# Kernel optimization log

Measured on AMD Instinct MI355X. Metric: run time of the kernel, lower is better.

The kernel has to match this reference:

```python
import jax, jax.numpy as jnp
import numpy as np

H = 1024  # hidden_size
NH = 16   # num_attention_heads
HD = H // NH  # head_dim = 64


def setup_inputs() -> dict:
    key = jax.random.key(0)
    ks = jax.random.split(key, 9)
    s = 0.02
    return {
        "hidden_states": jax.random.normal(ks[0], (2, 2048, H), dtype=jnp.float32),
        "Wq": jax.random.normal(ks[1], (H, H), dtype=jnp.float32) * s,
        "bq": jnp.zeros((H,), dtype=jnp.float32),
        "Wk": jax.random.normal(ks[2], (H, H), dtype=jnp.float32) * s,
        "bk": jnp.zeros((H,), dtype=jnp.float32),
        "Wv": jax.random.normal(ks[3], (H, H), dtype=jnp.float32) * s,
        "bv": jnp.zeros((H,), dtype=jnp.float32),
        "Wo": jax.random.normal(ks[4], (H, H), dtype=jnp.float32) * s,
        "bo": jnp.zeros((H,), dtype=jnp.float32),
    }


def reference(hidden_states, Wq, bq, Wk, bk, Wv, bv, Wo, bo):
    B, S, _ = hidden_states.shape
    scale = 1.0 / np.sqrt(HD)
    # torch Linear: x @ W.T + b
    q = (hidden_states @ Wq.T + bq).reshape(B, S, NH, HD).transpose(0, 2, 1, 3)
    k = (hidden_states @ Wk.T + bk).reshape(B, S, NH, HD).transpose(0, 2, 1, 3)
    v = (hidden_states @ Wv.T + bv).reshape(B, S, NH, HD).transpose(0, 2, 1, 3)
    # full (non-causal) attention; tiled_matmul == plain matmul mathematically
    scores = jnp.einsum("bhqd,bhkd->bhqk", q, k) * scale
    attn = jax.nn.softmax(scores, axis=-1)
    out = jnp.einsum("bhqk,bhkd->bhqd", attn, v)
    out = out.transpose(0, 2, 1, 3).reshape(B, S, H)
    return out @ Wo.T + bo
```

## Files before the change

kernel.cpp:

```cpp
#include <hip/hip_runtime.h>

typedef unsigned short u16;
typedef __attribute__((ext_vector_type(8))) short bf16x8;
typedef __attribute__((ext_vector_type(4))) float f32x4;
typedef __attribute__((ext_vector_type(4))) unsigned int u32x4;

#define SEQ 2048
#define HID 1024
#define NHEAD 16
#define HDIM 64
#define MTOK 4096

#define MFMA16(a,b,c) __builtin_amdgcn_mfma_f32_16x16x32_bf16(a,b,c,0,0,0)

__device__ __forceinline__ u16 f2bf(float f){
  unsigned int u = __builtin_bit_cast(unsigned int, f);
  u += 0x7fffu + ((u >> 16) & 1u);
  return (u16)(u >> 16);
}

__device__ __forceinline__ void gload16(const u16* g, u16* l){
  __builtin_amdgcn_global_load_lds((const __attribute__((address_space(1))) void*)g,
                                   (__attribute__((address_space(3))) void*)l, 16, 0, 0);
}

__global__ __launch_bounds__(256) void cast_f32_bf16(const float* __restrict__ in,
                                                     u16* __restrict__ out, int n8){
  int i = blockIdx.x * 256 + threadIdx.x;
  if (i >= n8) return;
  const float4* p = (const float4*)in;
  float4 a = p[2*i], b = p[2*i+1];
  u32x4 o;
  o.x = (unsigned)f2bf(a.x) | ((unsigned)f2bf(a.y) << 16);
  o.y = (unsigned)f2bf(a.z) | ((unsigned)f2bf(a.w) << 16);
  o.z = (unsigned)f2bf(b.x) | ((unsigned)f2bf(b.y) << 16);
  o.w = (unsigned)f2bf(b.z) | ((unsigned)f2bf(b.w) << 16);
  ((u32x4*)out)[i] = o;
}

__global__ __launch_bounds__(256) void cast_w4(const float* __restrict__ Wq,
                                               const float* __restrict__ Wk,
                                               const float* __restrict__ Wv,
                                               const float* __restrict__ Wo,
                                               u16* __restrict__ Wqkv, u16* __restrict__ Wob){
  int which = blockIdx.y;
  const float* src = (which == 0) ? Wq : (which == 1) ? Wk : (which == 2) ? Wv : Wo;
  u16* dst = (which == 3) ? Wob : (Wqkv + (size_t)which * HID * HID);
  int i = blockIdx.x * 256 + threadIdx.x;
  const float4* p = (const float4*)src;
  float4 a = p[2*i], b = p[2*i+1];
  u32x4 o;
  o.x = (unsigned)f2bf(a.x) | ((unsigned)f2bf(a.y) << 16);
  o.y = (unsigned)f2bf(a.z) | ((unsigned)f2bf(a.w) << 16);
  o.z = (unsigned)f2bf(b.x) | ((unsigned)f2bf(b.y) << 16);
  o.w = (unsigned)f2bf(b.z) | ((unsigned)f2bf(b.w) << 16);
  ((u32x4*)dst)[i] = o;
}

#define STAGE_G(Ag, Bg, k0, buf) do { \
  _Pragma("unroll") \
  for (int i_ = 0; i_ < 2; i_++){ \
    int u_ = (i_*4 + wave) * 64 + lane; \
    int row_ = u_ >> 2, cu_ = u_ & 3; \
    gload16(Ag + (size_t)(m0 + row_) * HID + (k0) + cu_*8, &As[buf][(i_*4 + wave) * 512]); \
    gload16(Bg + (size_t)(n0 + row_) * HID + (k0) + cu_*8, &Bs[buf][(i_*4 + wave) * 512]); \
  } } while(0)

__global__ __launch_bounds__(256) void gemm_qkv(
    const u16* __restrict__ Xb, const u16* __restrict__ Wqkv,
    const float* __restrict__ bq, const float* __restrict__ bk, const float* __restrict__ bv,
    u16* __restrict__ Qb, u16* __restrict__ Kb, u16* __restrict__ Vtb)
{
  __shared__ __attribute__((aligned(16))) u16 As[2][128*32];
  __shared__ __attribute__((aligned(16))) u16 Bs[2][128*32];
  const int tid = threadIdx.x, wave = tid >> 6, lane = tid & 63;
  const int m0 = blockIdx.x * 128, n0 = blockIdx.y * 128;
  const int wr = (wave >> 1) * 64, wc = (wave & 1) * 64;
  const int lr = lane & 15, lg = lane >> 4, kseg = lg * 8;

  f32x4 zero = {0.f, 0.f, 0.f, 0.f};
  f32x4 acc[4][4];
#pragma unroll
  for (int i = 0; i < 4; i++)
#pragma unroll
    for (int j = 0; j < 4; j++) acc[i][j] = zero;

  STAGE_G(Xb, Wqkv, 0, 0);
  for (int t = 0; t < 32; t++){
    int cur = t & 1;
    asm volatile("s_waitcnt vmcnt(0)" ::: "memory");
    __builtin_amdgcn_s_barrier();
    __builtin_amdgcn_sched_barrier(0);
    if (t < 31) STAGE_G(Xb, Wqkv, (t+1)*32, cur ^ 1);
    const u16* Ac = As[cur]; const u16* Bc = Bs[cur];
    bf16x8 af[4], bfr[4];
#pragma unroll
    for (int m = 0; m < 4; m++) af[m]  = *(const bf16x8*)&Ac[(wr + m*16 + lr)*32 + kseg];
#pragma unroll
    for (int n = 0; n < 4; n++) bfr[n] = *(const bf16x8*)&Bc[(wc + n*16 + lr)*32 + kseg];
    __builtin_amdgcn_s_setprio(1);
#pragma unroll
    for (int m = 0; m < 4; m++)
#pragma unroll
      for (int n = 0; n < 4; n++)
        acc[m][n] = MFMA16(af[m], bfr[n], acc[m][n]);
    __builtin_amdgcn_s_setprio(0);
  }

  const int sel = n0 >> 10;
  const float* bias = (sel == 0) ? bq : (sel == 1) ? bk : bv;
  const float qscale = (sel == 0) ? 0.18033688011f : 1.0f;
#pragma unroll
  for (int n = 0; n < 4; n++){
    int col = n0 + wc + n*16 + lr;
    int o = col & 1023;
    float bb = bias[o];
    int h = o >> 6, d = o & 63;
#pragma unroll
    for (int m = 0; m < 4; m++){
      int rbase = m0 + wr + m*16 + lg*4;
#pragma unroll
      for (int r = 0; r < 4; r++){
        int rowg = rbase + r;
        int b = rowg >> 11, s = rowg & 2047;
        u16 v = f2bf((acc[m][n][r] + bb) * qscale);
        if (sel == 0)      Qb [(((size_t)(b*16 + h))*SEQ + s)*HDIM + d] = v;
        else if (sel == 1) Kb [(((size_t)(b*16 + h))*SEQ + s)*HDIM + d] = v;
        else               Vtb[(((size_t)(b*16 + h))*HDIM + d)*SEQ + s] = v;
      }
    }
  }
}

__global__ __launch_bounds__(256) void attn_kernel(
    const u16* __restrict__ Qb, const u16* __restrict__ Kb, const u16* __restrict__ Vtb,
    u16* __restrict__ AOb)
{
  __shared__ __attribute__((aligned(16))) u16 Ks[2][64*64];
  __shared__ __attribute__((aligned(16))) u16 Vs[2][64*64];
  const int tid = threadIdx.x, wave = tid >> 6, lane = tid & 63;
  const int lr = lane & 15, lg = lane >> 4;
  const int bh = blockIdx.y;
  const int q0 = blockIdx.x * 128;
  const u16* Qh = Qb  + (size_t)bh * SEQ * HDIM;
  const u16* Kh = Kb  + (size_t)bh * SEQ * HDIM;
  const u16* Vh = Vtb + (size_t)bh * HDIM * SEQ;

#define STAGE_KV(kv0, buf) do { \
  _Pragma("unroll") \
  for (int i_ = 0; i_ < 2; i_++){ \
    int u_ = i_*256 + tid; \
    int r_ = u_ >> 3, s_ = u_ & 7, ss_ = s_ ^ (r_ & 7); \
    gload16(Kh + (size_t)((kv0) + r_) * HDIM + ss_*8, &Ks[buf][u_*8]); \
    gload16(Vh + (size_t)r_ * SEQ + (kv0) + ss_*8,    &Vs[buf][u_*8]); \
  } } while(0)

  bf16x8 qf[2][2];
#pragma unroll
  for (int qb = 0; qb < 2; qb++)
#pragma unroll
    for (int ks = 0; ks < 2; ks++)
      qf[qb][ks] = *(const bf16x8*)&Qh[(size_t)(q0 + wave*32 + qb*16 + lr) * HDIM + ks*32 + lg*8];

  f32x4 zero = {0.f, 0.f, 0.f, 0.f};
  f32x4 acc[2][4];
#pragma unroll
  for (int qb = 0; qb < 2; qb++)
#pragma unroll
    for (int fd = 0; fd < 4; fd++) acc[qb][fd] = zero;
  float m_c[2] = {-1e30f, -1e30f};
  float l_c[2] = {0.f, 0.f};

  STAGE_KV(0, 0);
  for (int t = 0; t < 32; t++){
    int cur = t & 1;
    asm volatile("s_waitcnt vmcnt(0)" ::: "memory");
    __builtin_amdgcn_s_barrier();
    __builtin_amdgcn_sched_barrier(0);
    if (t < 31) STAGE_KV((t+1)*64, cur ^ 1);
    const u16* Kc = &Ks[cur][0];
    const u16* Vc = &Vs[cur][0];

    f32x4 st[2][4];
    __builtin_amdgcn_s_setprio(1);
#pragma unroll
    for (int f = 0; f < 4; f++){
      bf16x8 kf0 = *(const bf16x8*)&Kc[(f*16 + lr)*64 + ((lg     ^ (lr & 7)) * 8)];
      bf16x8 kf1 = *(const bf16x8*)&Kc[(f*16 + lr)*64 + (((4+lg) ^ (lr & 7)) * 8)];
      st[0][f] = MFMA16(kf0, qf[0][0], zero);
      st[0][f] = MFMA16(kf1, qf[0][1], st[0][f]);
      st[1][f] = MFMA16(kf0, qf[1][0], zero);
      st[1][f] = MFMA16(kf1, qf[1][1], st[1][f]);
    }
    __builtin_amdgcn_s_setprio(0);

    float pm0, pm1;
    {
      float a0 = fmaxf(fmaxf(st[0][0][0], st[0][0][1]), fmaxf(st[0][0][2], st[0][0][3]));
      float a1 = fmaxf(fmaxf(st[0][1][0], st[0][1][1]), fmaxf(st[0][1][2], st[0][1][3]));
      float a2 = fmaxf(fmaxf(st[0][2][0], st[0][2][1]), fmaxf(st[0][2][2], st[0][2][3]));
      float a3 = fmaxf(fmaxf(st[0][3][0], st[0][3][1]), fmaxf(st[0][3][2], st[0][3][3]));
      pm0 = fmaxf(fmaxf(a0, a1), fmaxf(a2, a3));
      float b0 = fmaxf(fmaxf(st[1][0][0], st[1][0][1]), fmaxf(st[1][0][2], st[1][0][3]));
      float b1 = fmaxf(fmaxf(st[1][1][0], st[1][1][1]), fmaxf(st[1][1][2], st[1][1][3]));
      float b2 = fmaxf(fmaxf(st[1][2][0], st[1][2][1]), fmaxf(st[1][2][2], st[1][2][3]));
      float b3 = fmaxf(fmaxf(st[1][3][0], st[1][3][1]), fmaxf(st[1][3][2], st[1][3][3]));
      pm1 = fmaxf(fmaxf(b0, b1), fmaxf(b2, b3));
    }
    int need = (pm0 > m_c[0] + 11.5f) || (pm1 > m_c[1] + 11.5f);
    if (__any(need)){
#pragma unroll
      for (int qb = 0; qb < 2; qb++){
        float mt = (qb == 0) ? pm0 : pm1;
        mt = fmaxf(mt, __shfl_xor(mt, 16));
        mt = fmaxf(mt, __shfl_xor(mt, 32));
        float mn = fmaxf(m_c[qb], mt);
        float al = __builtin_amdgcn_exp2f(m_c[qb] - mn);
        m_c[qb] = mn;
        l_c[qb] *= al;
        float a0 = __shfl(al, lg*4 + 0), a1 = __shfl(al, lg*4 + 1);
        float a2 = __shfl(al, lg*4 + 2), a3 = __shfl(al, lg*4 + 3);
#pragma unroll
        for (int fd = 0; fd < 4; fd++){
          acc[qb][fd][0] *= a0; acc[qb][fd][1] *= a1;
          acc[qb][fd][2] *= a2; acc[qb][fd][3] *= a3;
        }
      }
    }

    bf16x8 pa[2][2];
#pragma unroll
    for (int qb = 0; qb < 2; qb++){
      unsigned w[4][2];
      float ssum = 0.f;
#pragma unroll
      for (int f = 0; f < 4; f++){
        float p0 = __builtin_amdgcn_exp2f(st[qb][f][0] - m_c[qb]);
        float p1 = __builtin_amdgcn_exp2f(st[qb][f][1] - m_c[qb]);
        float p2 = __builtin_amdgcn_exp2f(st[qb][f][2] - m_c[qb]);
        float p3 = __builtin_amdgcn_exp2f(st[qb][f][3] - m_c[qb]);
        ssum += (p0 + p1) + (p2 + p3);
        asm("v_cvt_pk_bf16_f32 %0, %1, %2" : "=v"(w[f][0]) : "v"(p0), "v"(p1));
        asm("v_cvt_pk_bf16_f32 %0, %1, %2" : "=v"(w[f][1]) : "v"(p2), "v"(p3));
      }
      l_c[qb] += ssum;
#pragma unroll
      for (int ks = 0; ks < 2; ks++){
        u32x4 aw;
#pragma unroll
        for (int rr = 0; rr < 2; rr++){
          unsigned X = w[2*ks][rr], Y = w[2*ks+1][rr];
          asm("v_permlane32_swap_b32 %0, %1" : "+v"(X), "+v"(Y));
          asm("v_permlane16_swap_b32 %0, %1" : "+v"(X), "+v"(Y));
          aw[rr] = X; aw[2 + rr] = Y;
        }
        pa[qb][ks] = __builtin_bit_cast(bf16x8, aw);
      }
    }

    __builtin_amdgcn_s_setprio(1);
#pragma unroll
    for (int ks = 0; ks < 2; ks++)
#pragma unroll
      for (int fd = 0; fd < 4; fd++){
        bf16x8 vf = *(const bf16x8*)&Vc[(fd*16 + lr)*64 + (((ks*4 + lg) ^ (lr & 7)) * 8)];
        acc[0][fd] = MFMA16(pa[0][ks], vf, acc[0][fd]);
        acc[1][fd] = MFMA16(pa[1][ks], vf, acc[1][fd]);
      }
    __builtin_amdgcn_s_setprio(0);
  }

  const int b = bh >> 4, h = bh & 15;
#pragma unroll
  for (int qb = 0; qb < 2; qb++){
    float lt = l_c[qb];
    lt += __shfl_xor(lt, 16);
    lt += __shfl_xor(lt, 32);
    float li[4];
#pragma unroll
    for (int r = 0; r < 4; r++) li[r] = 1.0f / __shfl(lt, lg*4 + r);
#pragma unroll
    for (int fd = 0; fd < 4; fd++){
      int d = h*64 + fd*16 + lr;
#pragma unroll
      for (int r = 0; r < 4; r++){
        int s = q0 + wave*32 + qb*16 + lg*4 + r;
        AOb[((size_t)(b*SEQ + s))*HID + d] = f2bf(acc[qb][fd][r] * li[r]);
      }
    }
  }
}

__global__ __launch_bounds__(256) void gemm_out(
    const u16* __restrict__ Ab, const u16* __restrict__ Wob,
    const float* __restrict__ bo, float* __restrict__ Out)
{
  __shared__ __attribute__((aligned(16))) u16 As[2][128*32];
  __shared__ __attribute__((aligned(16))) u16 Bs[2][128*32];
  const int tid = threadIdx.x, wave = tid >> 6, lane = tid & 63;
  const int m0 = blockIdx.x * 128, n0 = blockIdx.y * 128;
  const int wr = (wave >> 1) * 64, wc = (wave & 1) * 64;
  const int lr = lane & 15, lg = lane >> 4, kseg = lg * 8;

  f32x4 zero = {0.f, 0.f, 0.f, 0.f};
  f32x4 acc[4][4];
#pragma unroll
  for (int i = 0; i < 4; i++)
#pragma unroll
    for (int j = 0; j < 4; j++) acc[i][j] = zero;

  STAGE_G(Ab, Wob, 0, 0);
  for (int t = 0; t < 32; t++){
    int cur = t & 1;
    asm volatile("s_waitcnt vmcnt(0)" ::: "memory");
    __builtin_amdgcn_s_barrier();
    __builtin_amdgcn_sched_barrier(0);
    if (t < 31) STAGE_G(Ab, Wob, (t+1)*32, cur ^ 1);
    const u16* Ac = As[cur]; const u16* Bc = Bs[cur];
    bf16x8 af[4], bfr[4];
#pragma unroll
    for (int m = 0; m < 4; m++) af[m]  = *(const bf16x8*)&Ac[(wr + m*16 + lr)*32 + kseg];
#pragma unroll
    for (int n = 0; n < 4; n++) bfr[n] = *(const bf16x8*)&Bc[(wc + n*16 + lr)*32 + kseg];
    __builtin_amdgcn_s_setprio(1);
#pragma unroll
    for (int m = 0; m < 4; m++)
#pragma unroll
      for (int n = 0; n < 4; n++)
        acc[m][n] = MFMA16(af[m], bfr[n], acc[m][n]);
    __builtin_amdgcn_s_setprio(0);
  }

#pragma unroll
  for (int n = 0; n < 4; n++){
    int col = n0 + wc + n*16 + lr;
    float bb = bo[col];
#pragma unroll
    for (int m = 0; m < 4; m++){
      int rbase = m0 + wr + m*16 + lg*4;
#pragma unroll
      for (int r = 0; r < 4; r++)
        Out[(size_t)(rbase + r) * HID + col] = acc[m][n][r] + bb;
    }
  }
}

extern "C" void kernel_launch(void* const* d_in, const int* in_sizes, int n_in,
                              void* d_out, int out_size, void* d_ws, size_t ws_size,
                              hipStream_t stream){
  const float* hs = (const float*)d_in[0];
  const float* Wq = (const float*)d_in[1];
  const float* bq = (const float*)d_in[2];
  const float* Wk = (const float*)d_in[3];
  const float* bk = (const float*)d_in[4];
  const float* Wv = (const float*)d_in[5];
  const float* bv = (const float*)d_in[6];
  const float* Wo = (const float*)d_in[7];
  const float* bo = (const float*)d_in[8];
  float* Out = (float*)d_out;

  u16* Xb   = (u16*)d_ws;
  u16* Wqkv = Xb   + (size_t)MTOK * HID;
  u16* Wob  = Wqkv + (size_t)3 * HID * HID;
  u16* Qb   = Wob  + (size_t)HID * HID;
  u16* Kb   = Qb   + (size_t)MTOK * HID;
  u16* Vtb  = Kb   + (size_t)MTOK * HID;
  u16* AOb  = Vtb  + (size_t)MTOK * HID;

  cast_f32_bf16<<<2048, 256, 0, stream>>>(hs, Xb, MTOK * HID / 8);
  cast_w4<<<dim3(HID*HID/8/256, 4), 256, 0, stream>>>(Wq, Wk, Wv, Wo, Wqkv, Wob);

  gemm_qkv<<<dim3(MTOK/128, 3*HID/128), 256, 0, stream>>>(Xb, Wqkv, bq, bk, bv, Qb, Kb, Vtb);
  attn_kernel<<<dim3(SEQ/128, 2*NHEAD), 256, 0, stream>>>(Qb, Kb, Vtb, AOb);
  gemm_out<<<dim3(MTOK/128, HID/128), 256, 0, stream>>>(AOb, Wob, bo, Out);
}
```

Measured before the change: 208.9 us.

## Triple-buffer GEMM loads, halve attention and out-proj tiles, remap attention blocks per XCD

Both GEMMs move from double to triple buffered LDS staging and wait on partial vmcnt, so two tiles are in flight at once. The attention kernel now handles 64 queries per block (16 per wave) instead of 128. Its 1024 blocks are remapped so that each XCD works on 4 heads, which should keep K/V reuse inside one L2. The output GEMM uses 64x128 tiles to launch more blocks. Together these aim to raise occupancy and hide load latency, at the cost of more K/V re-reads per query and lower MFMA reuse per LDS load.

```diff
diff --git a/kernel.cpp b/kernel.cpp
--- a/kernel.cpp
+++ b/kernel.cpp
@@ -71,8 +71,8 @@
     const float* __restrict__ bq, const float* __restrict__ bk, const float* __restrict__ bv,
     u16* __restrict__ Qb, u16* __restrict__ Kb, u16* __restrict__ Vtb)
 {
-  __shared__ __attribute__((aligned(16))) u16 As[2][128*32];
-  __shared__ __attribute__((aligned(16))) u16 Bs[2][128*32];
+  __shared__ __attribute__((aligned(16))) u16 As[3][128*32];
+  __shared__ __attribute__((aligned(16))) u16 Bs[3][128*32];
   const int tid = threadIdx.x, wave = tid >> 6, lane = tid & 63;
   const int m0 = blockIdx.x * 128, n0 = blockIdx.y * 128;
   const int wr = (wave >> 1) * 64, wc = (wave & 1) * 64;
@@ -86,12 +86,14 @@
     for (int j = 0; j < 4; j++) acc[i][j] = zero;
 
   STAGE_G(Xb, Wqkv, 0, 0);
+  STAGE_G(Xb, Wqkv, 32, 1);
   for (int t = 0; t < 32; t++){
-    int cur = t & 1;
-    asm volatile("s_waitcnt vmcnt(0)" ::: "memory");
+    if (t < 31) { asm volatile("s_waitcnt vmcnt(4)" ::: "memory"); }
+    else        { asm volatile("s_waitcnt vmcnt(0)" ::: "memory"); }
     __builtin_amdgcn_s_barrier();
     __builtin_amdgcn_sched_barrier(0);
-    if (t < 31) STAGE_G(Xb, Wqkv, (t+1)*32, cur ^ 1);
+    if (t < 30) STAGE_G(Xb, Wqkv, (t+2)*32, (t+2)%3);
+    int cur = t % 3;
     const u16* Ac = As[cur]; const u16* Bc = Bs[cur];
     bf16x8 af[4], bfr[4];
 #pragma unroll
@@ -140,8 +142,10 @@
   __shared__ __attribute__((aligned(16))) u16 Vs[2][64*64];
   const int tid = threadIdx.x, wave = tid >> 6, lane = tid & 63;
   const int lr = lane & 15, lg = lane >> 4;
-  const int bh = blockIdx.y;
-  const int q0 = blockIdx.x * 128;
+  const int bid = blockIdx.x;
+  const int xcd = bid & 7, slot = bid >> 3;
+  const int bh = xcd*4 + (slot >> 5);
+  const int q0 = (slot & 31) * 64;
   const u16* Qh = Qb  + (size_t)bh * SEQ * HDIM;
   const u16* Kh = Kb  + (size_t)bh * SEQ * HDIM;
   const u16* Vh = Vtb + (size_t)bh * HDIM * SEQ;
@@ -155,21 +159,17 @@
     gload16(Vh + (size_t)r_ * SEQ + (kv0) + ss_*8,    &Vs[buf][u_*8]); \
   } } while(0)
 
-  bf16x8 qf[2][2];
-#pragma unroll
-  for (int qb = 0; qb < 2; qb++)
-#pragma unroll
-    for (int ks = 0; ks < 2; ks++)
-      qf[qb][ks] = *(const bf16x8*)&Qh[(size_t)(q0 + wave*32 + qb*16 + lr) * HDIM + ks*32 + lg*8];
+  bf16x8 qf[2];
+#pragma unroll
+  for (int ks = 0; ks < 2; ks++)
+    qf[ks] = *(const bf16x8*)&Qh[(size_t)(q0 + wave*16 + lr) * HDIM + ks*32 + lg*8];
 
   f32x4 zero = {0.f, 0.f, 0.f, 0.f};
-  f32x4 acc[2][4];
-#pragma unroll
-  for (int qb = 0; qb < 2; qb++)
-#pragma unroll
-    for (int fd = 0; fd < 4; fd++) acc[qb][fd] = zero;
-  float m_c[2] = {-1e30f, -1e30f};
-  float l_c[2] = {0.f, 0.f};
+  f32x4 acc[4];
+#pragma unroll
+  for (int fd = 0; fd < 4; fd++) acc[fd] = zero;
+  float m_c = -1e30f;
+  float l_c = 0.f;
 
   STAGE_KV(0, 0);
   for (int t = 0; t < 32; t++){
@@ -181,81 +181,64 @@
     const u16* Kc = &Ks[cur][0];
     const u16* Vc = &Vs[cur][0];
 
-    f32x4 st[2][4];
+    f32x4 st[4];
     __builtin_amdgcn_s_setprio(1);
 #pragma unroll
     for (int f = 0; f < 4; f++){
       bf16x8 kf0 = *(const bf16x8*)&Kc[(f*16 + lr)*64 + ((lg     ^ (lr & 7)) * 8)];
       bf16x8 kf1 = *(const bf16x8*)&Kc[(f*16 + lr)*64 + (((4+lg) ^ (lr & 7)) * 8)];
-      st[0][f] = MFMA16(kf0, qf[0][0], zero);
-      st[0][f] = MFMA16(kf1, qf[0][1], st[0][f]);
-      st[1][f] = MFMA16(kf0, qf[1][0], zero);
-      st[1][f] = MFMA16(kf1, qf[1][1], st[1][f]);
+      st[f] = MFMA16(kf0, qf[0], zero);
+      st[f] = MFMA16(kf1, qf[1], st[f]);
     }
     __builtin_amdgcn_s_setprio(0);
 
-    float pm0, pm1;
-    {
-      float a0 = fmaxf(fmaxf(st[0][0][0], st[0][0][1]), fmaxf(st[0][0][2], st[0][0][3]));
-      float a1 = fmaxf(fmaxf(st[0][1][0], st[0][1][1]), fmaxf(st[0][1][2], st[0][1][3]));
-      float a2 = fmaxf(fmaxf(st[0][2][0], st[0][2][1]), fmaxf(st[0][2][2], st[0][2][3]));
-      float a3 = fmaxf(fmaxf(st[0][3][0], st[0][3][1]), fmaxf(st[0][3][2], st[0][3][3]));
-      pm0 = fmaxf(fmaxf(a0, a1), fmaxf(a2, a3));
-      float b0 = fmaxf(fmaxf(st[1][0][0], st[1][0][1]), fmaxf(st[1][0][2], st[1][0][3]));
-      float b1 = fmaxf(fmaxf(st[1][1][0], st[1][1][1]), fmaxf(st[1][1][2], st[1][1][3]));
-      float b2 = fmaxf(fmaxf(st[1][2][0], st[1][2][1]), fmaxf(st[1][2][2], st[1][2][3]));
-      float b3 = fmaxf(fmaxf(st[1][3][0], st[1][3][1]), fmaxf(st[1][3][2], st[1][3][3]));
-      pm1 = fmaxf(fmaxf(b0, b1), fmaxf(b2, b3));
-    }
-    int need = (pm0 > m_c[0] + 11.5f) || (pm1 > m_c[1] + 11.5f);
-    if (__any(need)){
-#pragma unroll
-      for (int qb = 0; qb < 2; qb++){
-        float mt = (qb == 0) ? pm0 : pm1;
-        mt = fmaxf(mt, __shfl_xor(mt, 16));
-        mt = fmaxf(mt, __shfl_xor(mt, 32));
-        float mn = fmaxf(m_c[qb], mt);
-        float al = __builtin_amdgcn_exp2f(m_c[qb] - mn);
-        m_c[qb] = mn;
-        l_c[qb] *= al;
-        float a0 = __shfl(al, lg*4 + 0), a1 = __shfl(al, lg*4 + 1);
-        float a2 = __shfl(al, lg*4 + 2), a3 = __shfl(al, lg*4 + 3);
-#pragma unroll
-        for (int fd = 0; fd < 4; fd++){
-          acc[qb][fd][0] *= a0; acc[qb][fd][1] *= a1;
-          acc[qb][fd][2] *= a2; acc[qb][fd][3] *= a3;
-        }
+    float a0 = fmaxf(fmaxf(st[0][0], st[0][1]), fmaxf(st[0][2], st[0][3]));
+    float a1 = fmaxf(fmaxf(st[1][0], st[1][1]), fmaxf(st[1][2], st[1][3]));
+    float a2 = fmaxf(fmaxf(st[2][0], st[2][1]), fmaxf(st[2][2], st[2][3]));
+    float a3 = fmaxf(fmaxf(st[3][0], st[3][1]), fmaxf(st[3][2], st[3][3]));
+    float pm = fmaxf(fmaxf(a0, a1), fmaxf(a2, a3));
+    if (__any(pm > m_c + 11.5f)){
+      float mt = pm;
+      mt = fmaxf(mt, __shfl_xor(mt, 16));
+      mt = fmaxf(mt, __shfl_xor(mt, 32));
+      float mn = fmaxf(m_c, mt);
+      float al = __builtin_amdgcn_exp2f(m_c - mn);
+      m_c = mn;
+      l_c *= al;
+      float r0 = __shfl(al, lg*4 + 0), r1 = __shfl(al, lg*4 + 1);
+      float r2 = __shfl(al, lg*4 + 2), r3 = __shfl(al, lg*4 + 3);
+#pragma unroll
+      for (int fd = 0; fd < 4; fd++){
+        acc[fd][0] *= r0; acc[fd][1] *= r1;
+        acc[fd][2] *= r2; acc[fd][3] *= r3;
       }
     }
 
-    bf16x8 pa[2][2];
-#pragma unroll
-    for (int qb = 0; qb < 2; qb++){
-      unsigned w[4][2];
-      float ssum = 0.f;
-#pragma unroll
-      for (int f = 0; f < 4; f++){
-        float p0 = __builtin_amdgcn_exp2f(st[qb][f][0] - m_c[qb]);
-        float p1 = __builtin_amdgcn_exp2f(st[qb][f][1] - m_c[qb]);
-        float p2 = __builtin_amdgcn_exp2f(st[qb][f][2] - m_c[qb]);
-        float p3 = __builtin_amdgcn_exp2f(st[qb][f][3] - m_c[qb]);
-        ssum += (p0 + p1) + (p2 + p3);
-        asm("v_cvt_pk_bf16_f32 %0, %1, %2" : "=v"(w[f][0]) : "v"(p0), "v"(p1));
-        asm("v_cvt_pk_bf16_f32 %0, %1, %2" : "=v"(w[f][1]) : "v"(p2), "v"(p3));
+    unsigned w[4][2];
+    float ssum = 0.f;
+#pragma unroll
+    for (int f = 0; f < 4; f++){
+      float p0 = __builtin_amdgcn_exp2f(st[f][0] - m_c);
+      float p1 = __builtin_amdgcn_exp2f(st[f][1] - m_c);
+      float p2 = __builtin_amdgcn_exp2f(st[f][2] - m_c);
+      float p3 = __builtin_amdgcn_exp2f(st[f][3] - m_c);
+      ssum += (p0 + p1) + (p2 + p3);
+      asm("v_cvt_pk_bf16_f32 %0, %1, %2" : "=v"(w[f][0]) : "v"(p0), "v"(p1));
+      asm("v_cvt_pk_bf16_f32 %0, %1, %2" : "=v"(w[f][1]) : "v"(p2), "v"(p3));
+    }
+    l_c += ssum;
+    bf16x8 pa[2];
+#pragma unroll
+    for (int ks = 0; ks < 2; ks++){
+      u32x4 aw;
+#pragma unroll
+      for (int rr = 0; rr < 2; rr++){
+        unsigned X = w[2*ks][rr], Y = w[2*ks+1][rr];
+        asm("v_permlane32_swap_b32 %0, %1" : "+v"(X), "+v"(Y));
+        asm("v_permlane16_swap_b32 %0, %1" : "+v"(X), "+v"(Y));
+        aw[rr] = X; aw[2 + rr] = Y;
       }
-      l_c[qb] += ssum;
-#pragma unroll
-      for (int ks = 0; ks < 2; ks++){
-        u32x4 aw;
-#pragma unroll
-        for (int rr = 0; rr < 2; rr++){
-          unsigned X = w[2*ks][rr], Y = w[2*ks+1][rr];
-          asm("v_permlane32_swap_b32 %0, %1" : "+v"(X), "+v"(Y));
-          asm("v_permlane16_swap_b32 %0, %1" : "+v"(X), "+v"(Y));
-          aw[rr] = X; aw[2 + rr] = Y;
-        }
-        pa[qb][ks] = __builtin_bit_cast(bf16x8, aw);
-      }
+      pa[ks] = __builtin_bit_cast(bf16x8, aw);
     }
 
     __builtin_amdgcn_s_setprio(1);
@@ -264,29 +247,25 @@
 #pragma unroll
       for (int fd = 0; fd < 4; fd++){
         bf16x8 vf = *(const bf16x8*)&Vc[(fd*16 + lr)*64 + (((ks*4 + lg) ^ (lr & 7)) * 8)];
-        acc[0][fd] = MFMA16(pa[0][ks], vf, acc[0][fd]);
-        acc[1][fd] = MFMA16(pa[1][ks], vf, acc[1][fd]);
+        acc[fd] = MFMA16(pa[ks], vf, acc[fd]);
       }
     __builtin_amdgcn_s_setprio(0);
   }
 
   const int b = bh >> 4, h = bh & 15;
-#pragma unroll
-  for (int qb = 0; qb < 2; qb++){
-    float lt = l_c[qb];
-    lt += __shfl_xor(lt, 16);
-    lt += __shfl_xor(lt, 32);
-    float li[4];
-#pragma unroll
-    for (int r = 0; r < 4; r++) li[r] = 1.0f / __shfl(lt, lg*4 + r);
-#pragma unroll
-    for (int fd = 0; fd < 4; fd++){
-      int d = h*64 + fd*16 + lr;
-#pragma unroll
-      for (int r = 0; r < 4; r++){
-        int s = q0 + wave*32 + qb*16 + lg*4 + r;
-        AOb[((size_t)(b*SEQ + s))*HID + d] = f2bf(acc[qb][fd][r] * li[r]);
-      }
+  float lt = l_c;
+  lt += __shfl_xor(lt, 16);
+  lt += __shfl_xor(lt, 32);
+  float li[4];
+#pragma unroll
+  for (int r = 0; r < 4; r++) li[r] = 1.0f / __shfl(lt, lg*4 + r);
+#pragma unroll
+  for (int fd = 0; fd < 4; fd++){
+    int d = h*64 + fd*16 + lr;
+#pragma unroll
+    for (int r = 0; r < 4; r++){
+      int s = q0 + wave*16 + lg*4 + r;
+      AOb[((size_t)(b*SEQ + s))*HID + d] = f2bf(acc[fd][r] * li[r]);
     }
   }
 }
@@ -295,36 +274,49 @@
     const u16* __restrict__ Ab, const u16* __restrict__ Wob,
     const float* __restrict__ bo, float* __restrict__ Out)
 {
-  __shared__ __attribute__((aligned(16))) u16 As[2][128*32];
-  __shared__ __attribute__((aligned(16))) u16 Bs[2][128*32];
+  __shared__ __attribute__((aligned(16))) u16 As[3][64*32];
+  __shared__ __attribute__((aligned(16))) u16 Bs[3][128*32];
   const int tid = threadIdx.x, wave = tid >> 6, lane = tid & 63;
-  const int m0 = blockIdx.x * 128, n0 = blockIdx.y * 128;
-  const int wr = (wave >> 1) * 64, wc = (wave & 1) * 64;
+  const int m0 = blockIdx.x * 64, n0 = blockIdx.y * 128;
+  const int wr = (wave >> 1) * 32, wc = (wave & 1) * 64;
   const int lr = lane & 15, lg = lane >> 4, kseg = lg * 8;
 
+#define STAGE_O(k0, buf) do { \
+  { int u_ = wave*64 + lane; \
+    int row_ = u_ >> 2, cu_ = u_ & 3; \
+    gload16(Ab + (size_t)(m0 + row_) * HID + (k0) + cu_*8, &As[buf][wave * 512]); } \
+  _Pragma("unroll") \
+  for (int i_ = 0; i_ < 2; i_++){ \
+    int u_ = (i_*4 + wave) * 64 + lane; \
+    int row_ = u_ >> 2, cu_ = u_ & 3; \
+    gload16(Wob + (size_t)(n0 + row_) * HID + (k0) + cu_*8, &Bs[buf][(i_*4 + wave) * 512]); \
+  } } while(0)
+
   f32x4 zero = {0.f, 0.f, 0.f, 0.f};
-  f32x4 acc[4][4];
-#pragma unroll
-  for (int i = 0; i < 4; i++)
+  f32x4 acc[2][4];
+#pragma unroll
+  for (int i = 0; i < 2; i++)
 #pragma unroll
     for (int j = 0; j < 4; j++) acc[i][j] = zero;
 
-  STAGE_G(Ab, Wob, 0, 0);
+  STAGE_O(0, 0);
+  STAGE_O(32, 1);
   for (int t = 0; t < 32; t++){
-    int cur = t & 1;
-    asm volatile("s_waitcnt vmcnt(0)" ::: "memory");
+    if (t < 31) { asm volatile("s_waitcnt vmcnt(3)" ::: "memory"); }
+    else        { asm volatile("s_waitcnt vmcnt(0)" ::: "memory"); }
     __builtin_amdgcn_s_barrier();
     __builtin_amdgcn_sched_barrier(0);
-    if (t < 31) STAGE_G(Ab, Wob, (t+1)*32, cur ^ 1);
+    if (t < 30) STAGE_O((t+2)*32, (t+2)%3);
+    int cur = t % 3;
     const u16* Ac = As[cur]; const u16* Bc = Bs[cur];
-    bf16x8 af[4], bfr[4];
-#pragma unroll
-    for (int m = 0; m < 4; m++) af[m]  = *(const bf16x8*)&Ac[(wr + m*16 + lr)*32 + kseg];
+    bf16x8 af[2], bfr[4];
+#pragma unroll
+    for (int m = 0; m < 2; m++) af[m]  = *(const bf16x8*)&Ac[(wr + m*16 + lr)*32 + kseg];
 #pragma unroll
     for (int n = 0; n < 4; n++) bfr[n] = *(const bf16x8*)&Bc[(wc + n*16 + lr)*32 + kseg];
     __builtin_amdgcn_s_setprio(1);
 #pragma unroll
-    for (int m = 0; m < 4; m++)
+    for (int m = 0; m < 2; m++)
 #pragma unroll
       for (int n = 0; n < 4; n++)
         acc[m][n] = MFMA16(af[m], bfr[n], acc[m][n]);
@@ -336,7 +328,7 @@
     int col = n0 + wc + n*16 + lr;
     float bb = bo[col];
 #pragma unroll
-    for (int m = 0; m < 4; m++){
+    for (int m = 0; m < 2; m++){
       int rbase = m0 + wr + m*16 + lg*4;
 #pragma unroll
       for (int r = 0; r < 4; r++)
@@ -371,6 +363,6 @@
   cast_w4<<<dim3(HID*HID/8/256, 4), 256, 0, stream>>>(Wq, Wk, Wv, Wo, Wqkv, Wob);
 
   gemm_qkv<<<dim3(MTOK/128, 3*HID/128), 256, 0, stream>>>(Xb, Wqkv, bq, bk, bv, Qb, Kb, Vtb);
-  attn_kernel<<<dim3(SEQ/128, 2*NHEAD), 256, 0, stream>>>(Qb, Kb, Vtb, AOb);
-  gemm_out<<<dim3(MTOK/128, HID/128), 256, 0, stream>>>(AOb, Wob, bo, Out);
-}
+  attn_kernel<<<1024, 256, 0, stream>>>(Qb, Kb, Vtb, AOb);
+  gemm_out<<<dim3(MTOK/64, HID/128), 256, 0, stream>>>(AOb, Wob, bo, Out);
+}
```

New measurement: 211.1 us. No clear change (+1.0%).
